# Kernel optimization log

Hardware: AMD Instinct MI355X
Metric: run time of the kernel (lower is better)

Reference implementation:

```python
import jax, jax.numpy as jnp
import numpy as np

B, N, DIM = 2, 2048, 1024
H, KVH, DH = 16, 4, 64
SCALE = DH ** -0.5


def setup_inputs() -> dict:
    key = jax.random.key(0)
    ks = jax.random.split(key, 7)
    x = jax.random.normal(ks[0], (B, N, DIM), dtype=jnp.float32)
    mask = jax.random.randint(ks[1], (N, N), 0, 2).astype(jnp.bool_)
    Wq = jax.random.normal(ks[2], (DIM, H * DH), dtype=jnp.float32) * (DIM ** -0.5)
    Wk = jax.random.normal(ks[3], (DIM, KVH * DH), dtype=jnp.float32) * (DIM ** -0.5)
    Wv = jax.random.normal(ks[4], (DIM, KVH * DH), dtype=jnp.float32) * (DIM ** -0.5)
    Wo = jax.random.normal(ks[5], (H * DH, DIM), dtype=jnp.float32) * ((H * DH) ** -0.5)
    bo = jnp.zeros((DIM,), dtype=jnp.float32)
    return {"x": x, "mask": mask, "Wq": Wq, "Wk": Wk, "Wv": Wv, "Wo": Wo, "bo": bo}


def reference(x, mask, Wq, Wk, Wv, Wo, bo):
    b, n, _ = x.shape
    # projections -> [b, h, n, dh]
    q = (x @ Wq).reshape(b, n, H, DH).transpose(0, 2, 1, 3)
    k = (x @ Wk).reshape(b, n, KVH, DH).transpose(0, 2, 1, 3)
    v = (x @ Wv).reshape(b, n, KVH, DH).transpose(0, 2, 1, 3)
    # GQA: repeat kv heads, 'b h n d -> b (h r) n d'
    r = H // KVH
    k = jnp.repeat(k, r, axis=1)
    v = jnp.repeat(v, r, axis=1)
    dots = jnp.einsum('bhnd,bhmd->bhnm', q, k) * SCALE  # [b,h,n,n]
    dots = jnp.where(mask, jnp.float32(-1e9), dots)
    attn = jax.nn.softmax(dots, axis=-1)  # dropout p=0.0 -> identity
    out = jnp.einsum('bhnm,bhmd->bhnd', attn, v)
    out = out.transpose(0, 2, 1, 3).reshape(b, n, H * DH)
    return out @ Wo + bo
```

## Files before the change

### kernel.cpp

```cpp
#include <hip/hip_runtime.h>
#include <stdint.h>

typedef unsigned short u16;
typedef u16 u16x8 __attribute__((ext_vector_type(8)));
typedef u16 u16x4 __attribute__((ext_vector_type(4)));
typedef float f32x4 __attribute__((ext_vector_type(4)));

#define AS1(p) ((const __attribute__((address_space(1))) void*)(p))
#define AS3(p) ((__attribute__((address_space(3))) void*)(p))

__device__ __forceinline__ void gload16(void* lds, const void* g) {
  __builtin_amdgcn_global_load_lds(AS1(g), AS3(lds), 16, 0, 0);
}

__device__ __forceinline__ u16 f2bf(float f) {
  union { float f; uint32_t u; } c; c.f = f;
  uint32_t u = c.u + 0x7FFFu + ((c.u >> 16) & 1u);
  return (u16)(u >> 16);
}

__device__ __forceinline__ void mfma16(f32x4& d, u16x8 a, u16x8 b) {
  asm("v_mfma_f32_16x16x32_bf16 %0, %1, %2, %0" : "+v"(d) : "v"(a), "v"(b));
}


__global__ void cvt_x(const float* __restrict__ in, u16* __restrict__ out) {
  int i = (blockIdx.x * 256 + threadIdx.x) * 4;
  float4 v = *(const float4*)(in + i);
  u16x4 o; o.x = f2bf(v.x); o.y = f2bf(v.y); o.z = f2bf(v.z); o.w = f2bf(v.w);
  *(u16x4*)(out + i) = o;
}

__global__ void tconv(const float* __restrict__ in, u16* __restrict__ out, int R, int C) {
  __shared__ float t[64][65];
  const int c0 = blockIdx.x * 64, r0 = blockIdx.y * 64;
  const int tid = threadIdx.x;
#pragma unroll
  for (int k = 0; k < 4; ++k) {
    int idx = k * 256 + tid;
    int r = idx >> 4, c = (idx & 15) * 4;
    float4 v = *(const float4*)(in + (size_t)(r0 + r) * C + c0 + c);
    t[r][c] = v.x; t[r][c + 1] = v.y; t[r][c + 2] = v.z; t[r][c + 3] = v.w;
  }
  __syncthreads();
#pragma unroll
  for (int k = 0; k < 4; ++k) {
    int idx = k * 256 + tid;
    int c = idx >> 4, r = (idx & 15) * 4;
    u16x4 o;
    o.x = f2bf(t[r][c]); o.y = f2bf(t[r + 1][c]);
    o.z = f2bf(t[r + 2][c]); o.w = f2bf(t[r + 3][c]);
    *(u16x4*)(out + (size_t)(c0 + c) * R + r0 + r) = o;
  }
}

__global__ void mask_pack(const void* __restrict__ mraw, unsigned long long* __restrict__ bits) {
  const int lane = threadIdx.x & 63;
  const uint32_t* mi = (const uint32_t*)mraw;
  const bool int_mode = __all(mi[lane] <= 1u);
  const int wid = (blockIdx.x * 256 + threadIdx.x) >> 6;
  const size_t base = (size_t)(wid >> 5) * 2048 + (size_t)(wid & 31) * 64 + lane;
  bool bit;
  if (int_mode) bit = mi[base] != 0;
  else          bit = ((const uint8_t*)mraw)[base] != 0;
  unsigned long long b = __ballot(bit);
  if (lane == 0) bits[wid] = b;
}

#define SCALE_LOG2 0.18033688011112042f

template <int EPI>
__global__ __launch_bounds__(256, 2) void gemm_bt(
    const u16* __restrict__ A, const u16* __restrict__ Bt,
    u16* __restrict__ Qb, u16* __restrict__ Kb, u16* __restrict__ VTb,
    float* __restrict__ Co, const float* __restrict__ bias) {
  __shared__ u16 As[128 * 32];
  __shared__ u16 Bs[128 * 32];
  const int tid = threadIdx.x, lane = tid & 63, wave = tid >> 6;
  const int wr = wave >> 1, wc = wave & 1;
  const int lg = lane >> 4, ll = lane & 15;
  const int bm = blockIdx.x * 128, bn = blockIdx.y * 128;
  const int K = 1024;
  const u16* Ag = A + (size_t)bm * K;
  const u16* Bg = Bt + (size_t)bn * K;

  f32x4 acc[4][4];
#pragma unroll
  for (int m = 0; m < 4; ++m)
#pragma unroll
    for (int n = 0; n < 4; ++n) acc[m][n] = f32x4{0.f, 0.f, 0.f, 0.f};

  const int r0 = tid >> 2, c0 = (tid & 3) * 8;
  const int r1 = (256 + tid) >> 2;

  for (int k0 = 0; k0 < K; k0 += 32) {
    gload16(&As[(size_t)tid * 8],        Ag + (size_t)r0 * K + k0 + c0);
    gload16(&As[(size_t)(256 + tid) * 8], Ag + (size_t)r1 * K + k0 + c0);
    gload16(&Bs[(size_t)tid * 8],        Bg + (size_t)r0 * K + k0 + c0);
    gload16(&Bs[(size_t)(256 + tid) * 8], Bg + (size_t)r1 * K + k0 + c0);
    __syncthreads();
    u16x8 af[4], bf[4];
#pragma unroll
    for (int m = 0; m < 4; ++m) af[m] = *(const u16x8*)&As[(wr * 64 + m * 16 + ll) * 32 + lg * 8];
#pragma unroll
    for (int n = 0; n < 4; ++n) bf[n] = *(const u16x8*)&Bs[(wc * 64 + n * 16 + ll) * 32 + lg * 8];
#pragma unroll
    for (int m = 0; m < 4; ++m)
#pragma unroll
      for (int n = 0; n < 4; ++n) mfma16(acc[m][n], af[m], bf[n]);
    __syncthreads();
  }

  const int row0 = bm + wr * 64 + lg * 4;
  const int col0 = bn + wc * 64 + ll;
#pragma unroll
  for (int m = 0; m < 4; ++m) {
#pragma unroll
    for (int n = 0; n < 4; ++n) {
      const int col = col0 + n * 16;
#pragma unroll
      for (int r = 0; r < 4; ++r) {
        const int row = row0 + m * 16 + r;
        const float v = acc[m][n][r];
        if (EPI == 0) {
          const int b = row >> 11, t = row & 2047;
          if (col < 1024) {
            Qb[((size_t)(b * 16 + (col >> 6)) * 2048 + t) * 64 + (col & 63)] = f2bf(v * SCALE_LOG2);
          } else if (col < 1280) {
            const int c2 = col - 1024;
            Kb[((size_t)(b * 4 + (c2 >> 6)) * 2048 + t) * 64 + (c2 & 63)] = f2bf(v);
          } else {
            const int c2 = col - 1280;
            VTb[((size_t)(b * 4 + (c2 >> 6)) * 64 + (c2 & 63)) * 2048 + t] = f2bf(v);
          }
        } else {
          Co[(size_t)row * 1024 + col] = v + bias[col];
        }
      }
    }
  }
}


__device__ __forceinline__ void stage_kv(u16* Kl, u16* Vl,
                                         const u16* Kg, const u16* Vg,
                                         int kv0, int tid) {
  const int i0 = tid, i1 = 256 + tid;
  const int ra = i0 >> 3, sa = (i0 & 7) ^ (ra & 7);
  const int rb = i1 >> 3, sb = (i1 & 7) ^ (rb & 7);
  gload16(&Kl[(size_t)i0 * 8], Kg + (size_t)(kv0 + ra) * 64 + sa * 8);
  gload16(&Kl[(size_t)i1 * 8], Kg + (size_t)(kv0 + rb) * 64 + sb * 8);
  gload16(&Vl[(size_t)i0 * 8], Vg + (size_t)ra * 2048 + kv0 + sa * 8);
  gload16(&Vl[(size_t)i1 * 8], Vg + (size_t)rb * 2048 + kv0 + sb * 8);
}

__global__ __launch_bounds__(256, 2) void attn(
    const u16* __restrict__ Qb, const u16* __restrict__ Kb, const u16* __restrict__ VTb,
    const unsigned long long* __restrict__ mb, u16* __restrict__ Ob) {
  __shared__ u16 Klds[2][64 * 64];
  __shared__ u16 Vlds[2][64 * 64];
  __shared__ u16 Plds[4][32 * 64];
  const int tid = threadIdx.x, lane = tid & 63, wave = tid >> 6;
  const int lg = lane >> 4, ll = lane & 15;
  const int qt = blockIdx.x, h = blockIdx.y, b = blockIdx.z;
  const int kvh = h >> 2;
  const u16* Qg = Qb + ((size_t)(b * 16 + h) * 2048 + qt * 128 + wave * 32) * 64;
  const u16* Kg = Kb + (size_t)(b * 4 + kvh) * 2048 * 64;
  const u16* Vg = VTb + (size_t)(b * 4 + kvh) * 64 * 2048;
  u16* Pw = Plds[wave];
  const int sw = (ll & 7) << 3;

  u16x8 qf[2][2];
#pragma unroll
  for (int qb2 = 0; qb2 < 2; ++qb2)
#pragma unroll
    for (int kc = 0; kc < 2; ++kc)
      qf[qb2][kc] = *(const u16x8*)&Qg[(qb2 * 16 + ll) * 64 + kc * 32 + lg * 8];

  f32x4 o[2][4];
#pragma unroll
  for (int qb2 = 0; qb2 < 2; ++qb2)
#pragma unroll
    for (int db = 0; db < 4; ++db) o[qb2][db] = f32x4{0.f, 0.f, 0.f, 0.f};
  float mx[2] = {-3e9f, -3e9f}, ls[2] = {0.f, 0.f};
  const int qrow0 = qt * 128 + wave * 32;

  stage_kv(Klds[0], Vlds[0], Kg, Vg, 0, tid);

  for (int c = 0; c < 32; ++c) {
    const int cur = c & 1;
    const u16* Kl = Klds[cur];
    const u16* Vl = Vlds[cur];
    const unsigned long long w0 = mb[(size_t)(qrow0 + ll) * 32 + c];
    const unsigned long long w1 = mb[(size_t)(qrow0 + 16 + ll) * 32 + c];
    if (c < 31) {
      stage_kv(Klds[cur ^ 1], Vlds[cur ^ 1], Kg, Vg, (c + 1) * 64, tid);
      asm volatile("s_waitcnt vmcnt(4)" ::: "memory");
    } else {
      asm volatile("s_waitcnt vmcnt(0)" ::: "memory");
    }
    __builtin_amdgcn_s_barrier();
    asm volatile("" ::: "memory");

    f32x4 sf[2][4];
#pragma unroll
    for (int qb2 = 0; qb2 < 2; ++qb2)
#pragma unroll
      for (int kt = 0; kt < 4; ++kt) sf[qb2][kt] = f32x4{0.f, 0.f, 0.f, 0.f};
#pragma unroll
    for (int kt = 0; kt < 4; ++kt) {
      const int krow = kt * 16 + ll;
#pragma unroll
      for (int kc = 0; kc < 2; ++kc) {
        u16x8 kf = *(const u16x8*)&Kl[(krow * 64 + kc * 32 + lg * 8) ^ ((krow & 7) << 3)];
        mfma16(sf[0][kt], kf, qf[0][kc]);
        mfma16(sf[1][kt], kf, qf[1][kc]);
      }
    }

    float p[2][4][4], smax[2];
#pragma unroll
    for (int qb2 = 0; qb2 < 2; ++qb2) {
      const unsigned long long w = qb2 ? w1 : w0;
      float m0 = -3e9f;
#pragma unroll
      for (int kt = 0; kt < 4; ++kt)
#pragma unroll
        for (int r = 0; r < 4; ++r) {
          float s = sf[qb2][kt][r];
          s = ((w >> (kt * 16 + lg * 4 + r)) & 1ull) ? -3e9f : s;
          p[qb2][kt][r] = s;
          m0 = fmaxf(m0, s);
        }
      m0 = fmaxf(m0, __shfl_xor(m0, 16));
      m0 = fmaxf(m0, __shfl_xor(m0, 32));
      smax[qb2] = m0;
    }

    const bool upd = (smax[0] > mx[0] + 8.f) || (smax[1] > mx[1] + 8.f);
    if (__any(upd)) {
      float av[2];
#pragma unroll
      for (int qb2 = 0; qb2 < 2; ++qb2) {
        const float mn = fmaxf(mx[qb2], smax[qb2]);
        av[qb2] = exp2f(mx[qb2] - mn);
        mx[qb2] = mn;
        ls[qb2] *= av[qb2];
      }
#pragma unroll
      for (int r = 0; r < 4; ++r) {
        const float a0 = __shfl(av[0], lg * 4 + r);
        const float a1 = __shfl(av[1], lg * 4 + r);
#pragma unroll
        for (int db = 0; db < 4; ++db) { o[0][db][r] *= a0; o[1][db][r] *= a1; }
      }
    }

#pragma unroll
    for (int qb2 = 0; qb2 < 2; ++qb2) {
      const int q = qb2 * 16 + ll;
      float psum = 0.f;
#pragma unroll
      for (int kt = 0; kt < 4; ++kt) {
        float e0 = exp2f(p[qb2][kt][0] - mx[qb2]);
        float e1 = exp2f(p[qb2][kt][1] - mx[qb2]);
        float e2 = exp2f(p[qb2][kt][2] - mx[qb2]);
        float e3 = exp2f(p[qb2][kt][3] - mx[qb2]);
        psum += (e0 + e1) + (e2 + e3);
        u16x4 pk; pk.x = f2bf(e0); pk.y = f2bf(e1); pk.z = f2bf(e2); pk.w = f2bf(e3);
        *(u16x4*)&Pw[q * 64 + ((kt * 16 + lg * 4) ^ sw)] = pk;
      }
      psum += __shfl_xor(psum, 16);
      psum += __shfl_xor(psum, 32);
      ls[qb2] += psum;
    }

    asm volatile("" ::: "memory");
    __builtin_amdgcn_sched_barrier(0);

#pragma unroll
    for (int kc = 0; kc < 2; ++kc) {
      u16x8 pf[2];
#pragma unroll
      for (int qb2 = 0; qb2 < 2; ++qb2) {
        const int q = qb2 * 16 + ll;
        pf[qb2] = *(const u16x8*)&Pw[q * 64 + ((kc * 32 + lg * 8) ^ sw)];
      }
#pragma unroll
      for (int db = 0; db < 4; ++db) {
        const int d = db * 16 + ll;
        u16x8 vf = *(const u16x8*)&Vl[(d * 64 + kc * 32 + lg * 8) ^ ((d & 7) << 3)];
        mfma16(o[0][db], pf[0], vf);
        mfma16(o[1][db], pf[1], vf);
      }
    }
    asm volatile("s_waitcnt lgkmcnt(0)" ::: "memory");
    __builtin_amdgcn_s_barrier();
    asm volatile("" ::: "memory");
  }

#pragma unroll
  for (int qb2 = 0; qb2 < 2; ++qb2) {
#pragma unroll
    for (int r = 0; r < 4; ++r) {
      const float lsr = __shfl(ls[qb2], lg * 4 + r);
      const float inv = 1.f / lsr;
      const int tok = qt * 128 + wave * 32 + qb2 * 16 + lg * 4 + r;
#pragma unroll
      for (int db = 0; db < 4; ++db)
        Ob[(size_t)(b * 2048 + tok) * 1024 + h * 64 + db * 16 + ll] = f2bf(o[qb2][db][r] * inv);
    }
  }
}

extern "C" void kernel_launch(void* const* d_in, const int* in_sizes, int n_in,
                              void* d_out, int out_size, void* d_ws, size_t ws_size,
                              hipStream_t stream) {
  const float* x  = (const float*)d_in[0];
  const void*  mk = d_in[1];
  const float* Wq = (const float*)d_in[2];
  const float* Wk = (const float*)d_in[3];
  const float* Wv = (const float*)d_in[4];
  const float* Wo = (const float*)d_in[5];
  const float* bo = (const float*)d_in[6];
  float* out = (float*)d_out;

  char* ws = (char*)d_ws;
  size_t off = 0;
  auto alloc = [&](size_t bytes) { void* p = ws + off; off += (bytes + 255) & ~(size_t)255; return p; };
  u16* xb   = (u16*)alloc(4096ull * 1024 * 2);
  u16* Wcat = (u16*)alloc(1536ull * 1024 * 2);
  u16* WoT  = (u16*)alloc(1024ull * 1024 * 2);
  u16* Qb   = (u16*)alloc(2ull * 16 * 2048 * 64 * 2);
  u16* Kb   = (u16*)alloc(2ull * 4 * 2048 * 64 * 2);
  u16* VTb  = (u16*)alloc(2ull * 4 * 64 * 2048 * 2);
  u16* Ob   = (u16*)alloc(4096ull * 1024 * 2);
  unsigned long long* mbits = (unsigned long long*)alloc(65536ull * 8);
  (void)ws_size; (void)in_sizes; (void)n_in; (void)out_size;

  cvt_x<<<4096, 256, 0, stream>>>(x, xb);
  tconv<<<dim3(16, 16), 256, 0, stream>>>(Wq, Wcat, 1024, 1024);
  tconv<<<dim3(4, 16), 256, 0, stream>>>(Wk, Wcat + 1024 * 1024, 1024, 256);
  tconv<<<dim3(4, 16), 256, 0, stream>>>(Wv, Wcat + 1280 * 1024, 1024, 256);
  tconv<<<dim3(16, 16), 256, 0, stream>>>(Wo, WoT, 1024, 1024);
  mask_pack<<<16384, 256, 0, stream>>>(mk, mbits);

  gemm_bt<0><<<dim3(32, 12), 256, 0, stream>>>(xb, Wcat, Qb, Kb, VTb, nullptr, nullptr);
  attn<<<dim3(16, 16, 2), 256, 0, stream>>>(Qb, Kb, VTb, mbits, Ob);
  gemm_bt<1><<<dim3(32, 8), 256, 0, stream>>>(Ob, WoT, nullptr, nullptr, nullptr, out, bo);
}
```

Before: 176.6 us.

## Merge preprocessing kernels into one launch and shrink GEMM tiles for more blocks

The six preprocessing launches (x conversion, four weight transposes, mask packing) become one kernel that dispatches on block index, which removes launch gaps. The projection GEMMs are templated on tile size: QKV uses 64x128 tiles (768 blocks) and the output GEMM uses 128x64 tiles (512 blocks), so more blocks fill the CUs. Smaller tiles lower per-block data reuse, and every prep block now reserves the transpose shared-memory buffer.

```diff
diff --git a/kernel.cpp b/kernel.cpp
--- a/kernel.cpp
+++ b/kernel.cpp
@@ -23,100 +23,108 @@
   asm("v_mfma_f32_16x16x32_bf16 %0, %1, %2, %0" : "+v"(d) : "v"(a), "v"(b));
 }
 
-
-__global__ void cvt_x(const float* __restrict__ in, u16* __restrict__ out) {
-  int i = (blockIdx.x * 256 + threadIdx.x) * 4;
-  float4 v = *(const float4*)(in + i);
-  u16x4 o; o.x = f2bf(v.x); o.y = f2bf(v.y); o.z = f2bf(v.z); o.w = f2bf(v.w);
-  *(u16x4*)(out + i) = o;
-}
-
-__global__ void tconv(const float* __restrict__ in, u16* __restrict__ out, int R, int C) {
+__global__ void prep(const float* __restrict__ x, u16* __restrict__ xb,
+                     const void* __restrict__ mraw, unsigned long long* __restrict__ mb,
+                     const float* __restrict__ Wq, const float* __restrict__ Wk,
+                     const float* __restrict__ Wv, const float* __restrict__ Wo,
+                     u16* __restrict__ Wcat, u16* __restrict__ WoT) {
   __shared__ float t[64][65];
-  const int c0 = blockIdx.x * 64, r0 = blockIdx.y * 64;
-  const int tid = threadIdx.x;
-#pragma unroll
-  for (int k = 0; k < 4; ++k) {
-    int idx = k * 256 + tid;
-    int r = idx >> 4, c = (idx & 15) * 4;
-    float4 v = *(const float4*)(in + (size_t)(r0 + r) * C + c0 + c);
-    t[r][c] = v.x; t[r][c + 1] = v.y; t[r][c + 2] = v.z; t[r][c + 3] = v.w;
-  }
-  __syncthreads();
-#pragma unroll
-  for (int k = 0; k < 4; ++k) {
-    int idx = k * 256 + tid;
-    int c = idx >> 4, r = (idx & 15) * 4;
-    u16x4 o;
-    o.x = f2bf(t[r][c]); o.y = f2bf(t[r + 1][c]);
-    o.z = f2bf(t[r + 2][c]); o.w = f2bf(t[r + 3][c]);
-    *(u16x4*)(out + (size_t)(c0 + c) * R + r0 + r) = o;
-  }
-}
-
-__global__ void mask_pack(const void* __restrict__ mraw, unsigned long long* __restrict__ bits) {
-  const int lane = threadIdx.x & 63;
-  const uint32_t* mi = (const uint32_t*)mraw;
-  const bool int_mode = __all(mi[lane] <= 1u);
-  const int wid = (blockIdx.x * 256 + threadIdx.x) >> 6;
-  const size_t base = (size_t)(wid >> 5) * 2048 + (size_t)(wid & 31) * 64 + lane;
-  bool bit;
-  if (int_mode) bit = mi[base] != 0;
-  else          bit = ((const uint8_t*)mraw)[base] != 0;
-  unsigned long long b = __ballot(bit);
-  if (lane == 0) bits[wid] = b;
+  const int bi = blockIdx.x, tid = threadIdx.x;
+  if (bi < 4096) {
+    int i = (bi * 256 + tid) * 4;
+    float4 v = *(const float4*)(x + i);
+    u16x4 o; o.x = f2bf(v.x); o.y = f2bf(v.y); o.z = f2bf(v.z); o.w = f2bf(v.w);
+    *(u16x4*)(xb + i) = o;
+  } else if (bi < 20480) {
+    const int lane = tid & 63;
+    const uint32_t* mi = (const uint32_t*)mraw;
+    const bool int_mode = __all(mi[lane] <= 1u);
+    const int wid = ((bi - 4096) * 256 + tid) >> 6;
+    const size_t base = (size_t)(wid >> 5) * 2048 + (size_t)(wid & 31) * 64 + lane;
+    bool bit;
+    if (int_mode) bit = mi[base] != 0;
+    else          bit = ((const uint8_t*)mraw)[base] != 0;
+    unsigned long long bm = __ballot(bit);
+    if (lane == 0) mb[wid] = bm;
+  } else {
+    const float* in; u16* out; int R, C, bx, by, lb;
+    if (bi < 20736)      { lb = bi - 20480; in = Wq; out = Wcat;              R = 1024; C = 1024; bx = lb & 15; by = lb >> 4; }
+    else if (bi < 20800) { lb = bi - 20736; in = Wk; out = Wcat + 1024*1024;  R = 1024; C = 256;  bx = lb & 3;  by = lb >> 2; }
+    else if (bi < 20864) { lb = bi - 20800; in = Wv; out = Wcat + 1280*1024;  R = 1024; C = 256;  bx = lb & 3;  by = lb >> 2; }
+    else                 { lb = bi - 20864; in = Wo; out = WoT;               R = 1024; C = 1024; bx = lb & 15; by = lb >> 4; }
+    const int c0 = bx * 64, r0 = by * 64;
+#pragma unroll
+    for (int k = 0; k < 4; ++k) {
+      int idx = k * 256 + tid;
+      int r = idx >> 4, c = (idx & 15) * 4;
+      float4 v = *(const float4*)(in + (size_t)(r0 + r) * C + c0 + c);
+      t[r][c] = v.x; t[r][c + 1] = v.y; t[r][c + 2] = v.z; t[r][c + 3] = v.w;
+    }
+    __syncthreads();
+#pragma unroll
+    for (int k = 0; k < 4; ++k) {
+      int idx = k * 256 + tid;
+      int c = idx >> 4, r = (idx & 15) * 4;
+      u16x4 o;
+      o.x = f2bf(t[r][c]); o.y = f2bf(t[r + 1][c]);
+      o.z = f2bf(t[r + 2][c]); o.w = f2bf(t[r + 3][c]);
+      *(u16x4*)(out + (size_t)(c0 + c) * R + r0 + r) = o;
+    }
+  }
 }
 
 #define SCALE_LOG2 0.18033688011112042f
 
-template <int EPI>
+template <int EPI, int BM, int BN>
 __global__ __launch_bounds__(256, 2) void gemm_bt(
     const u16* __restrict__ A, const u16* __restrict__ Bt,
     u16* __restrict__ Qb, u16* __restrict__ Kb, u16* __restrict__ VTb,
     float* __restrict__ Co, const float* __restrict__ bias) {
-  __shared__ u16 As[128 * 32];
-  __shared__ u16 Bs[128 * 32];
+  constexpr int MR = BM / 32, NR = BN / 32;
+  __shared__ u16 As[BM * 32];
+  __shared__ u16 Bs[BN * 32];
   const int tid = threadIdx.x, lane = tid & 63, wave = tid >> 6;
   const int wr = wave >> 1, wc = wave & 1;
   const int lg = lane >> 4, ll = lane & 15;
-  const int bm = blockIdx.x * 128, bn = blockIdx.y * 128;
+  const int bm = blockIdx.x * BM, bn = blockIdx.y * BN;
   const int K = 1024;
   const u16* Ag = A + (size_t)bm * K;
   const u16* Bg = Bt + (size_t)bn * K;
 
-  f32x4 acc[4][4];
-#pragma unroll
-  for (int m = 0; m < 4; ++m)
-#pragma unroll
-    for (int n = 0; n < 4; ++n) acc[m][n] = f32x4{0.f, 0.f, 0.f, 0.f};
+  f32x4 acc[MR][NR];
+#pragma unroll
+  for (int m = 0; m < MR; ++m)
+#pragma unroll
+    for (int n = 0; n < NR; ++n) acc[m][n] = f32x4{0.f, 0.f, 0.f, 0.f};
 
   const int r0 = tid >> 2, c0 = (tid & 3) * 8;
-  const int r1 = (256 + tid) >> 2;
 
   for (int k0 = 0; k0 < K; k0 += 32) {
-    gload16(&As[(size_t)tid * 8],        Ag + (size_t)r0 * K + k0 + c0);
-    gload16(&As[(size_t)(256 + tid) * 8], Ag + (size_t)r1 * K + k0 + c0);
-    gload16(&Bs[(size_t)tid * 8],        Bg + (size_t)r0 * K + k0 + c0);
-    gload16(&Bs[(size_t)(256 + tid) * 8], Bg + (size_t)r1 * K + k0 + c0);
+    gload16(&As[(size_t)tid * 8], Ag + (size_t)r0 * K + k0 + c0);
+    if constexpr (BM == 128)
+      gload16(&As[(size_t)(256 + tid) * 8], Ag + (size_t)(64 + r0) * K + k0 + c0);
+    gload16(&Bs[(size_t)tid * 8], Bg + (size_t)r0 * K + k0 + c0);
+    if constexpr (BN == 128)
+      gload16(&Bs[(size_t)(256 + tid) * 8], Bg + (size_t)(64 + r0) * K + k0 + c0);
     __syncthreads();
-    u16x8 af[4], bf[4];
-#pragma unroll
-    for (int m = 0; m < 4; ++m) af[m] = *(const u16x8*)&As[(wr * 64 + m * 16 + ll) * 32 + lg * 8];
-#pragma unroll
-    for (int n = 0; n < 4; ++n) bf[n] = *(const u16x8*)&Bs[(wc * 64 + n * 16 + ll) * 32 + lg * 8];
-#pragma unroll
-    for (int m = 0; m < 4; ++m)
-#pragma unroll
-      for (int n = 0; n < 4; ++n) mfma16(acc[m][n], af[m], bf[n]);
+    u16x8 af[MR], bf[NR];
+#pragma unroll
+    for (int m = 0; m < MR; ++m) af[m] = *(const u16x8*)&As[(wr * (BM/2) + m * 16 + ll) * 32 + lg * 8];
+#pragma unroll
+    for (int n = 0; n < NR; ++n) bf[n] = *(const u16x8*)&Bs[(wc * (BN/2) + n * 16 + ll) * 32 + lg * 8];
+#pragma unroll
+    for (int m = 0; m < MR; ++m)
+#pragma unroll
+      for (int n = 0; n < NR; ++n) mfma16(acc[m][n], af[m], bf[n]);
     __syncthreads();
   }
 
-  const int row0 = bm + wr * 64 + lg * 4;
-  const int col0 = bn + wc * 64 + ll;
-#pragma unroll
-  for (int m = 0; m < 4; ++m) {
-#pragma unroll
-    for (int n = 0; n < 4; ++n) {
+  const int row0 = bm + wr * (BM/2) + lg * 4;
+  const int col0 = bn + wc * (BN/2) + ll;
+#pragma unroll
+  for (int m = 0; m < MR; ++m) {
+#pragma unroll
+    for (int n = 0; n < NR; ++n) {
       const int col = col0 + n * 16;
 #pragma unroll
       for (int r = 0; r < 4; ++r) {
@@ -338,14 +346,8 @@
   unsigned long long* mbits = (unsigned long long*)alloc(65536ull * 8);
   (void)ws_size; (void)in_sizes; (void)n_in; (void)out_size;
 
-  cvt_x<<<4096, 256, 0, stream>>>(x, xb);
-  tconv<<<dim3(16, 16), 256, 0, stream>>>(Wq, Wcat, 1024, 1024);
-  tconv<<<dim3(4, 16), 256, 0, stream>>>(Wk, Wcat + 1024 * 1024, 1024, 256);
-  tconv<<<dim3(4, 16), 256, 0, stream>>>(Wv, Wcat + 1280 * 1024, 1024, 256);
-  tconv<<<dim3(16, 16), 256, 0, stream>>>(Wo, WoT, 1024, 1024);
-  mask_pack<<<16384, 256, 0, stream>>>(mk, mbits);
-
-  gemm_bt<0><<<dim3(32, 12), 256, 0, stream>>>(xb, Wcat, Qb, Kb, VTb, nullptr, nullptr);
+  prep<<<21120, 256, 0, stream>>>(x, xb, mk, mbits, Wq, Wk, Wv, Wo, Wcat, WoT);
+  gemm_bt<0, 64, 128><<<dim3(64, 12), 256, 0, stream>>>(xb, Wcat, Qb, Kb, VTb, nullptr, nullptr);
   attn<<<dim3(16, 16, 2), 256, 0, stream>>>(Qb, Kb, VTb, mbits, Ob);
-  gemm_bt<1><<<dim3(32, 8), 256, 0, stream>>>(Ob, WoT, nullptr, nullptr, nullptr, out, bo);
-}
+  gemm_bt<1, 128, 64><<<dim3(32, 16), 256, 0, stream>>>(Ob, WoT, nullptr, nullptr, nullptr, out, bo);
+}
```

After: 157.5 us. 1.12x faster.
